# Optimization experiments

Hardware: AMD Instinct MI355X
Metric: run time of the kernel (lower is better)

## Reference

```python
import jax, jax.numpy as jnp
import numpy as np

NEG_INF = -9e15  # pygat masking constant
ALPHA = 0.2      # LeakyReLU slope


def _gat_head(h, adj_mask, W, a, concat):
    """One GraphAttentionLayer (pygat style).
    h: [b, N, Fin], adj_mask: [N, N] bool, W: [Fin, Fout], a: [2*Fout].
    """
    Fout = W.shape[1]
    Wh = jnp.einsum('bnf,fo->bno', h, W)              # [b, N, Fout]
    # e_ij = LeakyReLU(a_src . Wh_i + a_dst . Wh_j)
    e_src = Wh @ a[:Fout]                             # [b, N]
    e_dst = Wh @ a[Fout:]                             # [b, N]
    e = jax.nn.leaky_relu(e_src[:, :, None] + e_dst[:, None, :], ALPHA)  # [b, N, N]
    att = jax.nn.softmax(jnp.where(adj_mask, e, NEG_INF), axis=-1)
    out = jnp.einsum('bij,bjo->bio', att, Wh)         # [b, N, Fout]
    return jax.nn.elu(out) if concat else out


def setup_inputs() -> dict:
    key = jax.random.key(0)
    ks = jax.random.split(key, 8)
    b, N, F = 16384, 22, 192   # F = 3 * input_feature
    H = 192                    # 3 * hidden_feature (per head)
    x = jax.random.normal(ks[0], (b, N, F), dtype=jnp.float32)
    # symmetric binary adjacency with self loops (stand-in for skeleton graph A)
    u = jax.random.uniform(ks[1], (N, N))
    adj = ((u + u.T) < 0.8).astype(jnp.float32)
    adj = jnp.maximum(adj, jnp.eye(N, dtype=jnp.float32))
    s = 1.0 / np.sqrt(F)
    W1 = jax.random.normal(ks[2], (F, H), dtype=jnp.float32) * s
    a1 = jax.random.normal(ks[3], (2 * H,), dtype=jnp.float32) * s
    W2 = jax.random.normal(ks[4], (F, H), dtype=jnp.float32) * s
    a2 = jax.random.normal(ks[5], (2 * H,), dtype=jnp.float32) * s
    Wo = jax.random.normal(ks[6], (2 * H, F), dtype=jnp.float32) * (1.0 / np.sqrt(2 * H))
    ao = jax.random.normal(ks[7], (2 * F,), dtype=jnp.float32) * s
    return {"x": x, "adj": adj, "W1": W1, "a1": a1, "W2": W2, "a2": a2, "Wo": Wo, "ao": ao}


def reference(x, adj, W1, a1, W2, a2, Wo, ao):
    # ST_GCNA.forward: y = GAT(x_view, A) reshaped + residual x.
    # GAT (eval mode, dropout is identity): concat 2 heads, then elu(out_att).
    adj_mask = adj > 0
    h1 = _gat_head(x, adj_mask, W1, a1, concat=True)   # [b, N, H]
    h2 = _gat_head(x, adj_mask, W2, a2, concat=True)   # [b, N, H]
    hcat = jnp.concatenate([h1, h2], axis=-1)           # [b, N, 2H]
    y = jax.nn.elu(_gat_head(hcat, adj_mask, Wo, ao, concat=False))  # [b, N, F]
    return y + x
```

## Files before the change

### kernel.cpp

```cpp
#include <hip/hip_runtime.h>


typedef __attribute__((ext_vector_type(8))) short s16x8;
typedef __attribute__((ext_vector_type(4))) short s16x4;
typedef __attribute__((ext_vector_type(4))) float f32x4;

constexpr int NN = 22;
constexpr int FF = 192;
constexpr int AS = 200;
constexpr int TS = 40;

__device__ __forceinline__ short f2bf(float f) {
  union { float f; unsigned u; } v; v.f = f;
  unsigned r = v.u + 0x7FFFu + ((v.u >> 16) & 1u);
  return (short)(r >> 16);
}

__global__ void prep_vec(const float* __restrict__ W1, const float* __restrict__ a1,
                         const float* __restrict__ W2, const float* __restrict__ a2,
                         const float* __restrict__ Wo, const float* __restrict__ ao,
                         float* __restrict__ vecs) {
  int t = blockIdx.x * 256 + threadIdx.x;
  if (t >= 1536) return;
  const float* W; const float* a; int k;
  if (t < 384)      { W = W1; k = t % 192;            a = a1 + (t / 192) * 192; }
  else if (t < 768) { int u = t - 384; W = W2; k = u % 192; a = a2 + (u / 192) * 192; }
  else              { int u = t - 768; W = Wo; k = u % 384; a = ao + (u / 384) * 192; }
  float s = 0.f;
  for (int o = 0; o < 192; ++o) s += W[k * 192 + o] * a[o];
  vecs[t] = s;
}

__global__ void prep_pack(const float* __restrict__ W1, const float* __restrict__ W2,
                          const float* __restrict__ Wo, const float* __restrict__ vecs,
                          short* __restrict__ dst) {
  int idx = blockIdx.x * 256 + threadIdx.x;
  const float* W; int off, ksteps, v0, v1;
  if (idx < 39936)      { W = W1; off = 0;     ksteps = 6;  v0 = 0;   v1 = 192;  }
  else if (idx < 79872) { W = W2; off = 39936; ksteps = 6;  v0 = 384; v1 = 576;  }
  else                  { W = Wo; off = 79872; ksteps = 12; v0 = 768; v1 = 1152; }
  int local = idx - off;
  int j = local & 7, l = (local >> 3) & 63, fi = local >> 9;
  int nt = fi / ksteps, ks = fi - nt * ksteps;
  int k = ks * 32 + ((l >> 4) << 3) + j;
  int nl = l & 15;
  float v;
  if (nt < 12) v = W[k * 192 + nt * 16 + nl];
  else         v = (nl == 0) ? vecs[v0 + k] : (nl == 1) ? vecs[v1 + k] : 0.f;
  dst[idx] = f2bf(v);
}

struct Accs { f32x4 a[2][3]; f32x4 e[2]; };

__device__ __forceinline__ void zacc(Accs& a) {
  #pragma unroll
  for (int m = 0; m < 2; ++m) {
    #pragma unroll
    for (int t = 0; t < 3; ++t) a.a[m][t] = (f32x4){0.f, 0.f, 0.f, 0.f};
    a.e[m] = (f32x4){0.f, 0.f, 0.f, 0.f};
  }
}

__device__ __attribute__((always_inline)) inline void gemm6(
    const short* A, const s16x8* __restrict__ B, int ksTot, int ksOff,
    Accs& ac, int m0, int kg, int wave, int lane) {
  for (int ks = 0; ks < 6; ++ks) {
    const short* ap = A + ks * 32 + kg * 8;
    s16x8 av0 = *(const s16x8*)(ap + m0 * AS);
    s16x8 av1 = *(const s16x8*)(ap + (m0 + 16) * AS);
    #pragma unroll
    for (int t = 0; t < 3; ++t) {
      s16x8 bv = B[((wave * 3 + t) * ksTot + ksOff + ks) * 64 + lane];
      ac.a[0][t] = __builtin_amdgcn_mfma_f32_16x16x32_bf16(av0, bv, ac.a[0][t], 0, 0, 0);
      ac.a[1][t] = __builtin_amdgcn_mfma_f32_16x16x32_bf16(av1, bv, ac.a[1][t], 0, 0, 0);
    }
    if (wave == 3) {
      s16x8 bv = B[(12 * ksTot + ksOff + ks) * 64 + lane];
      ac.e[0] = __builtin_amdgcn_mfma_f32_16x16x32_bf16(av0, bv, ac.e[0], 0, 0, 0);
      ac.e[1] = __builtin_amdgcn_mfma_f32_16x16x32_bf16(av1, bv, ac.e[1], 0, 0, 0);
    }
  }
}

__device__ __attribute__((always_inline)) inline void storeD(
    const Accs& ac, short* WhTp, float* esp, float* edp, int m0, int kg, int wave) {
  #pragma unroll
  for (int m = 0; m < 2; ++m)
    #pragma unroll
    for (int t = 0; t < 3; ++t) {
      int col = (wave * 3 + t) * 16 + m0;
      int row0 = m * 16 + kg * 4;
      s16x4 p = { f2bf(ac.a[m][t][0]), f2bf(ac.a[m][t][1]),
                  f2bf(ac.a[m][t][2]), f2bf(ac.a[m][t][3]) };
      *(s16x4*)&WhTp[col * TS + row0] = p;
    }
  if (wave == 3 && m0 < 2) {
    float* dst = m0 ? edp : esp;
    #pragma unroll
    for (int m = 0; m < 2; ++m) {
      int row0 = m * 16 + kg * 4;
      #pragma unroll
      for (int r = 0; r < 4; ++r)
        if (row0 + r < NN) dst[row0 + r] = ac.e[m][r];
    }
  }
}

__device__ __attribute__((always_inline)) inline void pv22(
    const short* attAp, const short* WhTp, f32x4 pa[2][3], int m0, int kg, int wave) {
  s16x8 av0 = *(const s16x8*)(attAp + m0 * TS + kg * 8);
  s16x8 av1 = *(const s16x8*)(attAp + (m0 + 16) * TS + kg * 8);
  #pragma unroll
  for (int t = 0; t < 3; ++t) {
    int col = (wave * 3 + t) * 16 + m0;
    s16x8 bv = *(const s16x8*)(WhTp + col * TS + kg * 8);
    pa[0][t] = __builtin_amdgcn_mfma_f32_16x16x32_bf16(av0, bv, pa[0][t], 0, 0, 0);
    pa[1][t] = __builtin_amdgcn_mfma_f32_16x16x32_bf16(av1, bv, pa[1][t], 0, 0, 0);
  }
}

__global__ __launch_bounds__(256, 3) void gat_main(
    const float* __restrict__ x, const float* __restrict__ adj,
    const short* __restrict__ wsb, float* __restrict__ out) {
  __shared__ __align__(16) short As1[32 * AS];
  __shared__ __align__(16) short Ah [32 * AS];
  __shared__ __align__(16) short attA[32 * TS];
  __shared__ __align__(16) short WhT[FF * TS];
  __shared__ float es[NN], ed[NN];
  __shared__ unsigned adjm[NN];

  const int tid = threadIdx.x, lane = tid & 63, wave = tid >> 6;
  const int m0 = lane & 15, kg = (lane >> 4) & 3;
  const size_t b = blockIdx.x;
  const float* xb = x + b * (size_t)(NN * FF);

  for (int i4 = tid; i4 < 1056; i4 += 256) {
    int row = i4 / 48, c = (i4 - row * 48) * 4;
    float4 v = ((const float4*)xb)[i4];
    s16x4 p = { f2bf(v.x), f2bf(v.y), f2bf(v.z), f2bf(v.w) };
    *(s16x4*)&As1[row * AS + c] = p;
  }
  {
    int* z1 = (int*)(As1 + NN * AS);
    int* z2 = (int*)(Ah + NN * AS);
    for (int i = tid; i < 1000; i += 256) { z1[i] = 0; z2[i] = 0; }
  }
  if (tid < NN) {
    unsigned m = 0;
    for (int j = 0; j < NN; ++j) m |= (adj[tid * NN + j] > 0.f ? 1u : 0u) << j;
    adjm[tid] = m;
  }
  __syncthreads();

  const s16x8* BW  = (const s16x8*)wsb;
  const s16x8* BWo = (const s16x8*)wsb + 9984;

  Accs aco; zacc(aco);

  for (int h = 0; h < 2; ++h) {
    Accs ach; zacc(ach);
    gemm6(As1, BW + h * 4992, 6, 0, ach, m0, kg, wave, lane);
    storeD(ach, WhT, es, ed, m0, kg, wave);
    __syncthreads();

    if (tid < NN) {
      unsigned msk = adjm[tid];
      float esi = es[tid];
      float p[NN]; float mx = -3e38f;
      #pragma unroll
      for (int j = 0; j < NN; ++j) {
        float e = esi + ed[j];
        e = e > 0.f ? e : 0.2f * e;
        e = ((msk >> j) & 1) ? e : -9e15f;
        p[j] = e; mx = fmaxf(mx, e);
      }
      float sum = 0.f;
      #pragma unroll
      for (int j = 0; j < NN; ++j) { float q = __expf(p[j] - mx); p[j] = q; sum += q; }
      float inv = 1.f / sum;
      int* row = (int*)(attA + tid * TS);
      #pragma unroll
      for (int j2 = 0; j2 < 11; ++j2) {
        unsigned lo = (unsigned short)f2bf(p[2 * j2] * inv);
        unsigned hi = (unsigned short)f2bf(p[2 * j2 + 1] * inv);
        row[j2] = (int)(lo | (hi << 16));
      }
      #pragma unroll
      for (int j2 = 11; j2 < 16; ++j2) row[j2] = 0;
    }
    __syncthreads();

    f32x4 pa[2][3];
    #pragma unroll
    for (int m = 0; m < 2; ++m)
      #pragma unroll
      for (int t = 0; t < 3; ++t) pa[m][t] = (f32x4){0.f, 0.f, 0.f, 0.f};
    pv22(attA, WhT, pa, m0, kg, wave);
    #pragma unroll
    for (int m = 0; m < 2; ++m)
      #pragma unroll
      for (int t = 0; t < 3; ++t) {
        int col = (wave * 3 + t) * 16 + m0;
        int row0 = m * 16 + kg * 4;
        #pragma unroll
        for (int r = 0; r < 4; ++r) {
          int row = row0 + r;
          if (row < NN) {
            float v = pa[m][t][r];
            v = v > 0.f ? v : expm1f(v);
            Ah[row * AS + col] = f2bf(v);
          }
        }
      }
    __syncthreads();

    gemm6(Ah, BWo, 12, 6 * h, aco, m0, kg, wave, lane);
  }

  storeD(aco, WhT, es, ed, m0, kg, wave);
  __syncthreads();
  if (tid < NN) {
    unsigned msk = adjm[tid];
    float esi = es[tid];
    float p[NN]; float mx = -3e38f;
    #pragma unroll
    for (int j = 0; j < NN; ++j) {
      float e = esi + ed[j];
      e = e > 0.f ? e : 0.2f * e;
      e = ((msk >> j) & 1) ? e : -9e15f;
      p[j] = e; mx = fmaxf(mx, e);
    }
    float sum = 0.f;
    #pragma unroll
    for (int j = 0; j < NN; ++j) { float q = __expf(p[j] - mx); p[j] = q; sum += q; }
    float inv = 1.f / sum;
    int* row = (int*)(attA + tid * TS);
    #pragma unroll
    for (int j2 = 0; j2 < 11; ++j2) {
      unsigned lo = (unsigned short)f2bf(p[2 * j2] * inv);
      unsigned hi = (unsigned short)f2bf(p[2 * j2 + 1] * inv);
      row[j2] = (int)(lo | (hi << 16));
    }
    #pragma unroll
    for (int j2 = 11; j2 < 16; ++j2) row[j2] = 0;
  }
  __syncthreads();

  f32x4 pa[2][3];
  #pragma unroll
  for (int m = 0; m < 2; ++m)
    #pragma unroll
    for (int t = 0; t < 3; ++t) pa[m][t] = (f32x4){0.f, 0.f, 0.f, 0.f};
  pv22(attA, WhT, pa, m0, kg, wave);
  float* ob = out + b * (size_t)(NN * FF);
  #pragma unroll
  for (int m = 0; m < 2; ++m)
    #pragma unroll
    for (int t = 0; t < 3; ++t) {
      int col = (wave * 3 + t) * 16 + m0;
      int row0 = m * 16 + kg * 4;
      #pragma unroll
      for (int r = 0; r < 4; ++r) {
        int row = row0 + r;
        if (row < NN) {
          float v = pa[m][t][r];
          v = v > 0.f ? v : expm1f(v);
          ob[row * FF + col] = v + xb[row * FF + col];
        }
      }
    }
}

extern "C" void kernel_launch(void* const* d_in, const int* in_sizes, int n_in,
                              void* d_out, int out_size, void* d_ws, size_t ws_size,
                              hipStream_t stream) {
  const float* x   = (const float*)d_in[0];
  const float* adj = (const float*)d_in[1];
  const float* W1  = (const float*)d_in[2];
  const float* a1  = (const float*)d_in[3];
  const float* W2  = (const float*)d_in[4];
  const float* a2  = (const float*)d_in[5];
  const float* Wo  = (const float*)d_in[6];
  const float* ao  = (const float*)d_in[7];
  float* out = (float*)d_out;
  short* wsb  = (short*)d_ws;
  float* vecs = (float*)((char*)d_ws + 319488);

  const int batch = in_sizes[0] / (NN * FF);
  prep_vec <<<6,   256, 0, stream>>>(W1, a1, W2, a2, Wo, ao, vecs);
  prep_pack<<<624, 256, 0, stream>>>(W1, W2, Wo, vecs, wsb);
  gat_main <<<batch, 256, 0, stream>>>(x, adj, wsb, out);
}
```

Before: 1.110 ms.

## Parallelize softmax across 8 lanes per row and use hardware bf16 pack conversion

The 22-row attention softmax, which ran on one thread per row, is spread over 8 lanes per row with shuffle reductions, so it occupies 176 threads instead of 22. Manual bf16 rounding is replaced by the v_cvt_pk_bf16_f32 instruction, which packs two values per instruction. expm1f in ELU is replaced with __expf minus one, trading some accuracy near zero for fewer instructions. The goal is to shorten the serial softmax phase between barriers and cut ALU work in the conversions.

```diff
diff --git a/kernel.cpp b/kernel.cpp
--- a/kernel.cpp
+++ b/kernel.cpp
@@ -3,6 +3,7 @@
 
 typedef __attribute__((ext_vector_type(8))) short s16x8;
 typedef __attribute__((ext_vector_type(4))) short s16x4;
+typedef __attribute__((ext_vector_type(2))) int i32x2;
 typedef __attribute__((ext_vector_type(4))) float f32x4;
 
 constexpr int NN = 22;
@@ -14,6 +15,17 @@
   union { float f; unsigned u; } v; v.f = f;
   unsigned r = v.u + 0x7FFFu + ((v.u >> 16) & 1u);
   return (short)(r >> 16);
+}
+
+__device__ __forceinline__ int cvt_pk_bf16(float lo, float hi) {
+  int r;
+  asm("v_cvt_pk_bf16_f32 %0, %1, %2" : "=v"(r) : "v"(lo), "v"(hi));
+  return r;
+}
+
+__device__ __forceinline__ float elu1(float v) {
+  float e = __expf(v) - 1.0f;
+  return v > 0.f ? v : e;
 }
 
 __global__ void prep_vec(const float* __restrict__ W1, const float* __restrict__ a1,
@@ -90,9 +102,9 @@
     for (int t = 0; t < 3; ++t) {
       int col = (wave * 3 + t) * 16 + m0;
       int row0 = m * 16 + kg * 4;
-      s16x4 p = { f2bf(ac.a[m][t][0]), f2bf(ac.a[m][t][1]),
-                  f2bf(ac.a[m][t][2]), f2bf(ac.a[m][t][3]) };
-      *(s16x4*)&WhTp[col * TS + row0] = p;
+      i32x2 p = { cvt_pk_bf16(ac.a[m][t][0], ac.a[m][t][1]),
+                  cvt_pk_bf16(ac.a[m][t][2], ac.a[m][t][3]) };
+      *(i32x2*)&WhTp[col * TS + row0] = p;
     }
   if (wave == 3 && m0 < 2) {
     float* dst = m0 ? edp : esp;
@@ -104,6 +116,39 @@
         if (row0 + r < NN) dst[row0 + r] = ac.e[m][r];
     }
   }
+}
+
+__device__ __forceinline__ void softmax22(
+    const float* es, const float* ed, const unsigned* adjm, short* attA, int tid) {
+  int i = tid >> 3, jl = tid & 7;
+  if (i >= NN) return;
+  unsigned msk = adjm[i];
+  float esi = es[i];
+  float pv[3]; float mx = -3e38f;
+  #pragma unroll
+  for (int c = 0; c < 3; ++c) {
+    int j = jl + 8 * c;
+    int jc = j < NN ? j : 0;
+    float e = esi + ed[jc];
+    e = e > 0.f ? e : 0.2f * e;
+    bool live = (j < NN) && ((msk >> j) & 1u);
+    pv[c] = live ? e : -9e15f;
+    mx = fmaxf(mx, pv[c]);
+  }
+  #pragma unroll
+  for (int d = 1; d < 8; d <<= 1) mx = fmaxf(mx, __shfl_xor(mx, d, 8));
+  float s = 0.f;
+  #pragma unroll
+  for (int c = 0; c < 3; ++c) { float q = __expf(pv[c] - mx); pv[c] = q; s += q; }
+  #pragma unroll
+  for (int d = 1; d < 8; d <<= 1) s += __shfl_xor(s, d, 8);
+  float inv = 1.f / s;
+  #pragma unroll
+  for (int c = 0; c < 3; ++c) {
+    int j = jl + 8 * c;
+    if (j < 24) attA[i * TS + j] = (j < NN) ? f2bf(pv[c] * inv) : (short)0;
+  }
+  attA[i * TS + 24 + jl] = 0;
 }
 
 __device__ __attribute__((always_inline)) inline void pv22(
@@ -137,8 +182,8 @@
   for (int i4 = tid; i4 < 1056; i4 += 256) {
     int row = i4 / 48, c = (i4 - row * 48) * 4;
     float4 v = ((const float4*)xb)[i4];
-    s16x4 p = { f2bf(v.x), f2bf(v.y), f2bf(v.z), f2bf(v.w) };
-    *(s16x4*)&As1[row * AS + c] = p;
+    i32x2 p = { cvt_pk_bf16(v.x, v.y), cvt_pk_bf16(v.z, v.w) };
+    *(i32x2*)&As1[row * AS + c] = p;
   }
   {
     int* z1 = (int*)(As1 + NN * AS);
@@ -163,31 +208,7 @@
     storeD(ach, WhT, es, ed, m0, kg, wave);
     __syncthreads();
 
-    if (tid < NN) {
-      unsigned msk = adjm[tid];
-      float esi = es[tid];
-      float p[NN]; float mx = -3e38f;
-      #pragma unroll
-      for (int j = 0; j < NN; ++j) {
-        float e = esi + ed[j];
-        e = e > 0.f ? e : 0.2f * e;
-        e = ((msk >> j) & 1) ? e : -9e15f;
-        p[j] = e; mx = fmaxf(mx, e);
-      }
-      float sum = 0.f;
-      #pragma unroll
-      for (int j = 0; j < NN; ++j) { float q = __expf(p[j] - mx); p[j] = q; sum += q; }
-      float inv = 1.f / sum;
-      int* row = (int*)(attA + tid * TS);
-      #pragma unroll
-      for (int j2 = 0; j2 < 11; ++j2) {
-        unsigned lo = (unsigned short)f2bf(p[2 * j2] * inv);
-        unsigned hi = (unsigned short)f2bf(p[2 * j2 + 1] * inv);
-        row[j2] = (int)(lo | (hi << 16));
-      }
-      #pragma unroll
-      for (int j2 = 11; j2 < 16; ++j2) row[j2] = 0;
-    }
+    softmax22(es, ed, adjm, attA, tid);
     __syncthreads();
 
     f32x4 pa[2][3];
@@ -202,15 +223,13 @@
       for (int t = 0; t < 3; ++t) {
         int col = (wave * 3 + t) * 16 + m0;
         int row0 = m * 16 + kg * 4;
-        #pragma unroll
-        for (int r = 0; r < 4; ++r) {
-          int row = row0 + r;
-          if (row < NN) {
-            float v = pa[m][t][r];
-            v = v > 0.f ? v : expm1f(v);
-            Ah[row * AS + col] = f2bf(v);
-          }
-        }
+        float v0 = elu1(pa[m][t][0]), v1 = elu1(pa[m][t][1]);
+        float v2 = elu1(pa[m][t][2]), v3 = elu1(pa[m][t][3]);
+        int qa = cvt_pk_bf16(v0, v1), qb = cvt_pk_bf16(v2, v3);
+        if (row0 < NN)     Ah[row0 * AS + col]       = (short)qa;
+        if (row0 + 1 < NN) Ah[(row0 + 1) * AS + col] = (short)(qa >> 16);
+        if (row0 + 2 < NN) Ah[(row0 + 2) * AS + col] = (short)qb;
+        if (row0 + 3 < NN) Ah[(row0 + 3) * AS + col] = (short)(qb >> 16);
       }
     __syncthreads();
 
@@ -219,31 +238,7 @@
 
   storeD(aco, WhT, es, ed, m0, kg, wave);
   __syncthreads();
-  if (tid < NN) {
-    unsigned msk = adjm[tid];
-    float esi = es[tid];
-    float p[NN]; float mx = -3e38f;
-    #pragma unroll
-    for (int j = 0; j < NN; ++j) {
-      float e = esi + ed[j];
-      e = e > 0.f ? e : 0.2f * e;
-      e = ((msk >> j) & 1) ? e : -9e15f;
-      p[j] = e; mx = fmaxf(mx, e);
-    }
-    float sum = 0.f;
-    #pragma unroll
-    for (int j = 0; j < NN; ++j) { float q = __expf(p[j] - mx); p[j] = q; sum += q; }
-    float inv = 1.f / sum;
-    int* row = (int*)(attA + tid * TS);
-    #pragma unroll
-    for (int j2 = 0; j2 < 11; ++j2) {
-      unsigned lo = (unsigned short)f2bf(p[2 * j2] * inv);
-      unsigned hi = (unsigned short)f2bf(p[2 * j2 + 1] * inv);
-      row[j2] = (int)(lo | (hi << 16));
-    }
-    #pragma unroll
-    for (int j2 = 11; j2 < 16; ++j2) row[j2] = 0;
-  }
+  softmax22(es, ed, adjm, attA, tid);
   __syncthreads();
 
   f32x4 pa[2][3];
@@ -263,8 +258,7 @@
       for (int r = 0; r < 4; ++r) {
         int row = row0 + r;
         if (row < NN) {
-          float v = pa[m][t][r];
-          v = v > 0.f ? v : expm1f(v);
+          float v = elu1(pa[m][t][r]);
           ob[row * FF + col] = v + xb[row * FF + col];
         }
       }
```

After: 945.2 us. 14.8% less time.
